# Optimization experiments

Hardware: AMD Instinct MI355X
Metric: run time of the kernel (lower is better)

## Reference

```python
import jax, jax.numpy as jnp
import numpy as np

C = 512
H = 8
D = C // H
GROUPS = 32
EPS = 1e-5

def setup_inputs() -> dict:
    key = jax.random.key(0)
    ks = jax.random.split(key, 7)
    B, L = 4, 2048
    x = jax.random.normal(ks[0], (B, C, L), dtype=jnp.float32)
    gamma = jnp.ones((C,), dtype=jnp.float32)
    beta = jnp.zeros((C,), dtype=jnp.float32)
    w_qkv = jax.random.normal(ks[1], (3 * C, C), dtype=jnp.float32) * (1.0 / np.sqrt(C))
    b_qkv = jax.random.normal(ks[2], (3 * C,), dtype=jnp.float32) * 0.01
    w_proj = jax.random.normal(ks[3], (C, C), dtype=jnp.float32) * (1.0 / np.sqrt(C))
    b_proj = jax.random.normal(ks[4], (C,), dtype=jnp.float32) * 0.01
    return {"x": x, "gamma": gamma, "beta": beta, "w_qkv": w_qkv,
            "b_qkv": b_qkv, "w_proj": w_proj, "b_proj": b_proj}

def _group_norm(x, gamma, beta):
    B, Cc, L = x.shape
    xg = x.reshape(B, GROUPS, Cc // GROUPS, L)
    mean = jnp.mean(xg, axis=(2, 3), keepdims=True)
    var = jnp.var(xg, axis=(2, 3), keepdims=True)
    xn = ((xg - mean) * jax.lax.rsqrt(var + EPS)).reshape(B, Cc, L)
    return xn * gamma[None, :, None] + beta[None, :, None]

def reference(x, gamma, beta, w_qkv, b_qkv, w_proj, b_proj):
    B, Cc, L = x.shape
    h = _group_norm(x, gamma, beta)
    # 1x1 conv == channel matmul: (3C,C) x (B,C,L) -> (B,3C,L)
    qkv = jnp.einsum('oc,bcl->bol', w_qkv, h) + b_qkv[None, :, None]
    q, k, v = jnp.split(qkv, 3, axis=1)
    # (B,C,L) -> (B,H,L,D)
    def to_heads(t):
        return t.reshape(B, H, D, L).transpose(0, 1, 3, 2)
    q, k, v = to_heads(q), to_heads(k), to_heads(v)
    scale = 1.0 / np.sqrt(D).astype(np.float32)
    attn = jnp.einsum('bhqd,bhkd->bhqk', q, k) * scale  # [B,H,L,L]
    attn = jax.nn.softmax(attn, axis=-1)
    out = jnp.einsum('bhqk,bhkd->bhqd', attn, v)  # [B,H,L,D]
    out = out.transpose(0, 1, 3, 2).reshape(B, Cc, L)
    proj = jnp.einsum('oc,bcl->bol', w_proj, out) + b_proj[None, :, None]
    return x + proj
```

## Files before the change

kernel.cpp:

```cpp
#include <hip/hip_runtime.h>
#include <stdint.h>

#define C_DIM 512
#define H_HEADS 8
#define D_HEAD 64
#define B_BATCH 4
#define L_SEQ 2048
#define GROUPS 32
#define EPS_GN 1e-5f

typedef unsigned short u16;
typedef __attribute__((ext_vector_type(8))) __bf16 bf16x8;
typedef __attribute__((ext_vector_type(4))) float f32x4;
typedef __attribute__((ext_vector_type(16))) float f32x16;

__device__ __forceinline__ u16 f2bf(float f) {
  unsigned u = __builtin_bit_cast(unsigned, f);
  unsigned r = u + 0x7FFFu + ((u >> 16) & 1u);
  return (u16)(r >> 16);
}

__device__ __forceinline__ unsigned cvtpk_bf16(float lo, float hi) {
  unsigned r;
  asm("v_cvt_pk_bf16_f32 %0, %1, %2" : "=v"(r) : "v"(lo), "v"(hi));
  return r;
}

__device__ __forceinline__ void pl32swap(unsigned& a, unsigned& b) {
  asm("v_permlane32_swap_b32 %0, %1" : "+v"(a), "+v"(b));
}

__device__ __forceinline__ bf16x8 mk8(unsigned a, unsigned b, unsigned c, unsigned d) {
  union { uint4 u; bf16x8 v; } z;
  z.u.x = a; z.u.y = b; z.u.z = c; z.u.w = d;
  return z.v;
}

__device__ __forceinline__ void gl16(const void* g, void* l) {
  __builtin_amdgcn_global_load_lds((const __attribute__((address_space(1))) void*)g,
                                   (__attribute__((address_space(3))) void*)l, 16, 0, 0);
}

__global__ __launch_bounds__(256) void cvt_weights(const float* __restrict__ wq,
                                                   const float* __restrict__ wp,
                                                   u16* __restrict__ wq_bf,
                                                   u16* __restrict__ wp_bf) {
  int i = blockIdx.x * 256 + threadIdx.x;
  const int nq = 3 * C_DIM * C_DIM;
  int idx = i * 4;
  const float* src;
  u16* dst;
  if (idx < nq) { src = wq + idx; dst = wq_bf + idx; }
  else          { src = wp + (idx - nq); dst = wp_bf + (idx - nq); }
  float4 v = *(const float4*)src;
  uint2 pk;
  pk.x = (unsigned)f2bf(v.x) | ((unsigned)f2bf(v.y) << 16);
  pk.y = (unsigned)f2bf(v.z) | ((unsigned)f2bf(v.w) << 16);
  *(uint2*)dst = pk;
}

__global__ __launch_bounds__(256) void groupnorm_kernel(const float* __restrict__ x,
                                                        const float* __restrict__ gamma,
                                                        const float* __restrict__ beta,
                                                        u16* __restrict__ h_t) {
  int bg = blockIdx.x;
  int b = bg >> 5, g = bg & 31;
  const float* base = x + ((size_t)(b * C_DIM + g * 16)) * L_SEQ;
  int t = threadIdx.x;
  int w = t >> 6;
  float s = 0.f, sq = 0.f;
  for (int i = 0; i < 32; ++i) {
    float4 v = ((const float4*)base)[t + i * 256];
    s += v.x + v.y + v.z + v.w;
    sq += v.x * v.x + v.y * v.y + v.z * v.z + v.w * v.w;
  }
  for (int off = 32; off; off >>= 1) { s += __shfl_down(s, off); sq += __shfl_down(sq, off); }
  __shared__ float red[8];
  if ((t & 63) == 0) { red[w * 2] = s; red[w * 2 + 1] = sq; }
  __syncthreads();
  float ts = red[0] + red[2] + red[4] + red[6];
  float tq = red[1] + red[3] + red[5] + red[7];
  float mean = ts * (1.f / 32768.f);
  float var = tq * (1.f / 32768.f) - mean * mean;
  float rstd = rsqrtf(var + EPS_GN);
  float ga[16], be[16];
#pragma unroll
  for (int c = 0; c < 16; ++c) {
    float gm = gamma[g * 16 + c];
    ga[c] = gm * rstd;
    be[c] = beta[g * 16 + c] - mean * gm * rstd;
  }
  __shared__ float tile[16][260];
  for (int lc = 0; lc < 8; ++lc) {
    __syncthreads();
#pragma unroll
    for (int it = 0; it < 4; ++it) {
      int r = it * 4 + w;
      int c4 = (t & 63) * 4;
      *(float4*)&tile[r][c4] = *(const float4*)(base + (size_t)r * L_SEQ + lc * 256 + c4);
    }
    __syncthreads();
    int l = lc * 256 + t;
    unsigned wds[8];
#pragma unroll
    for (int c = 0; c < 8; ++c) {
      float a0 = tile[2 * c][t] * ga[2 * c] + be[2 * c];
      float a1 = tile[2 * c + 1][t] * ga[2 * c + 1] + be[2 * c + 1];
      wds[c] = (unsigned)f2bf(a0) | ((unsigned)f2bf(a1) << 16);
    }
    u16* dst = h_t + ((size_t)(b * L_SEQ + l)) * C_DIM + g * 16;
    uint4 p0; p0.x = wds[0]; p0.y = wds[1]; p0.z = wds[2]; p0.w = wds[3];
    uint4 p1; p1.x = wds[4]; p1.y = wds[5]; p1.z = wds[6]; p1.w = wds[7];
    *(uint4*)dst = p0;
    *(uint4*)(dst + 8) = p1;
  }
}

template <int MODE>
__global__ __launch_bounds__(256) void gemm_kernel(const u16* __restrict__ A_bf,
                                                   const u16* __restrict__ B_t,
                                                   const float* __restrict__ bias,
                                                   const float* __restrict__ xres,
                                                   u16* __restrict__ q_t,
                                                   u16* __restrict__ kf_g,
                                                   u16* __restrict__ vf_g,
                                                   float* __restrict__ out_f) {
  constexpr int K = 512;
  __shared__ u16 A_lds[128][32];
  __shared__ u16 B_lds[128][32];
  int t = threadIdx.x;
  int w = t >> 6, lane = t & 63;
  int q4 = lane >> 4, c15 = lane & 15;
  int wm = w >> 1, wn = w & 1;
  int o0 = blockIdx.y * 128;
  int l0 = blockIdx.x * 128;
  int b = blockIdx.z;
  const u16* Bb = B_t + (size_t)b * L_SEQ * K;
  f32x4 acc[4][4] = {};

  int sr = lane >> 2, sc = lane & 3;
  int r0 = w * 32 + sr;
  int r1 = r0 + 16;
  int lc0 = (sc - (r0 >> 1)) & 3;
  int lc1 = (sc - (r1 >> 1)) & 3;
  const u16* Ag0 = A_bf + (size_t)(o0 + r0) * K + lc0 * 8;
  const u16* Ag1 = A_bf + (size_t)(o0 + r1) * K + lc1 * 8;
  const u16* Bg0 = Bb + (size_t)(l0 + r0) * K + lc0 * 8;
  const u16* Bg1 = Bb + (size_t)(l0 + r1) * K + lc1 * 8;
  u16* Al0 = &A_lds[w * 32][0];
  u16* Al1 = &A_lds[w * 32 + 16][0];
  u16* Bl0 = &B_lds[w * 32][0];
  u16* Bl1 = &B_lds[w * 32 + 16][0];

  for (int kt = 0; kt < K / 32; ++kt) {
    gl16(Ag0, Al0); gl16(Ag1, Al1);
    gl16(Bg0, Bl0); gl16(Bg1, Bl1);
    Ag0 += 32; Ag1 += 32; Bg0 += 32; Bg1 += 32;
    __syncthreads();
    bf16x8 af[4], bfr[4];
#pragma unroll
    for (int mi = 0; mi < 4; ++mi) {
      int ar = wm * 64 + mi * 16 + c15;
      af[mi] = *(const bf16x8*)&A_lds[ar][((q4 + (ar >> 1)) & 3) * 8];
    }
#pragma unroll
    for (int ni = 0; ni < 4; ++ni) {
      int br = wn * 64 + ni * 16 + c15;
      bfr[ni] = *(const bf16x8*)&B_lds[br][((q4 + (br >> 1)) & 3) * 8];
    }
#pragma unroll
    for (int mi = 0; mi < 4; ++mi)
#pragma unroll
      for (int ni = 0; ni < 4; ++ni)
        acc[mi][ni] = __builtin_amdgcn_mfma_f32_16x16x32_bf16(af[mi], bfr[ni], acc[mi][ni], 0, 0, 0);
    __syncthreads();
  }

  if (MODE == 0) {
    const float QS = 0.18033688f;
    int sel = o0 >> 9;
    int ob = o0 - sel * 512 + wm * 64;
#pragma unroll
    for (int mi = 0; mi < 4; ++mi) {
      int orow = ob + mi * 16 + q4 * 4;
      float4 bi = *(const float4*)&bias[o0 + wm * 64 + mi * 16 + q4 * 4];
#pragma unroll
      for (int ni = 0; ni < 4; ++ni) {
        int l = l0 + wn * 64 + ni * 16 + c15;
        float v0 = acc[mi][ni][0] + bi.x;
        float v1 = acc[mi][ni][1] + bi.y;
        float v2 = acc[mi][ni][2] + bi.z;
        float v3 = acc[mi][ni][3] + bi.w;
        if (sel == 0) {
          v0 *= QS; v1 *= QS; v2 *= QS; v3 *= QS;
          uint2 pk;
          pk.x = (unsigned)f2bf(v0) | ((unsigned)f2bf(v1) << 16);
          pk.y = (unsigned)f2bf(v2) | ((unsigned)f2bf(v3) << 16);
          *(uint2*)(q_t + ((size_t)(b * L_SEQ + l)) * C_DIM + orow) = pk;
        } else if (sel == 1) {
          int hh = orow >> 6, d = orow & 63;
          size_t base = ((size_t)(b * 8 + hh)) * 131072 +
                        (size_t)(((l >> 5) * 4 + (d >> 4))) * 512 +
                        (size_t)((l & 31) + ((d >> 3) & 1) * 32) * 8 + (d & 7);
          uint2 pk;
          pk.x = (unsigned)f2bf(v0) | ((unsigned)f2bf(v1) << 16);
          pk.y = (unsigned)f2bf(v2) | ((unsigned)f2bf(v3) << 16);
          *(uint2*)(kf_g + base) = pk;
        } else {
          int hh = orow >> 6, d = orow & 63;
          size_t base0 = ((size_t)(b * 8 + hh)) * 131072 +
                         (size_t)(l >> 4) * 1024 +
                         (size_t)((l >> 3) & 1) * 256 + (l & 7);
          vf_g[base0 + (size_t)((d + 0) >> 5) * 512 + ((d + 0) & 31) * 8] = f2bf(v0);
          vf_g[base0 + (size_t)((d + 1) >> 5) * 512 + ((d + 1) & 31) * 8] = f2bf(v1);
          vf_g[base0 + (size_t)((d + 2) >> 5) * 512 + ((d + 2) & 31) * 8] = f2bf(v2);
          vf_g[base0 + (size_t)((d + 3) >> 5) * 512 + ((d + 3) & 31) * 8] = f2bf(v3);
        }
      }
    }
  } else {
#pragma unroll
    for (int mi = 0; mi < 4; ++mi) {
      int orow = o0 + wm * 64 + mi * 16 + q4 * 4;
      float4 bi = *(const float4*)&bias[orow];
#pragma unroll
      for (int ni = 0; ni < 4; ++ni) {
        int l = l0 + wn * 64 + ni * 16 + c15;
        size_t base2 = ((size_t)(b * C_DIM + orow)) * L_SEQ + l;
        out_f[base2] = acc[mi][ni][0] + bi.x + xres[base2];
        out_f[base2 + L_SEQ] = acc[mi][ni][1] + bi.y + xres[base2 + L_SEQ];
        out_f[base2 + 2 * L_SEQ] = acc[mi][ni][2] + bi.z + xres[base2 + 2 * L_SEQ];
        out_f[base2 + 3 * L_SEQ] = acc[mi][ni][3] + bi.w + xres[base2 + 3 * L_SEQ];
      }
    }
  }
}

#define ABODY(KL, KN, VC, SC, SN, T)                                           \
  {                                                                            \
    int tl = (T) + 2; tl = tl > TMAX ? TMAX : tl;                              \
    const u16* kp = kfb + tl * 2048;                                           \
    const u16* vp = vfb + tl * 2048;                                           \
    KL[0] = *(const bf16x8*)(kp);                                              \
    KL[1] = *(const bf16x8*)(kp + 512);                                        \
    KL[2] = *(const bf16x8*)(kp + 1024);                                       \
    KL[3] = *(const bf16x8*)(kp + 1536);                                       \
    _Pragma("unroll") for (int r = 0; r < 16; ++r) SN[r] = 0.f;                \
    _Pragma("unroll") for (int kk = 0; kk < 4; ++kk)                           \
        SN = __builtin_amdgcn_mfma_f32_32x32x16_bf16(KN[kk], qf[kk], SN, 0, 0, 0); \
    float mx = fmaxf(fmaxf(SC[0], SC[1]), SC[2]);                              \
    float m1 = fmaxf(fmaxf(SC[3], SC[4]), SC[5]);                              \
    float m2 = fmaxf(fmaxf(SC[6], SC[7]), SC[8]);                              \
    float m3 = fmaxf(fmaxf(SC[9], SC[10]), SC[11]);                            \
    float m4 = fmaxf(fmaxf(SC[12], SC[13]), SC[14]);                           \
    mx = fmaxf(fmaxf(mx, SC[15]), fmaxf(m1, m2));                              \
    mx = fmaxf(mx, fmaxf(m3, m4));                                             \
    mx = fmaxf(mx, __shfl_xor(mx, 32));                                        \
    float mnew = fmaxf(m_r, mx);                                               \
    float al = __builtin_amdgcn_exp2f(m_r - mnew);                             \
    m_r = mnew;                                                                \
    l_r *= al;                                                                 \
    _Pragma("unroll") for (int r = 0; r < 16; ++r) { o0[r] *= al; o1[r] *= al; } \
    _Pragma("unroll") for (int r = 0; r < 16; ++r)                             \
        SC[r] = __builtin_amdgcn_exp2f(SC[r] - m_r);                           \
    float s0 = (SC[0] + SC[1]) + (SC[2] + SC[3]);                              \
    float s1 = (SC[4] + SC[5]) + (SC[6] + SC[7]);                              \
    float s2 = (SC[8] + SC[9]) + (SC[10] + SC[11]);                            \
    float s3 = (SC[12] + SC[13]) + (SC[14] + SC[15]);                          \
    float sum = (s0 + s1) + (s2 + s3);                                         \
    sum += __shfl_xor(sum, 32);                                                \
    l_r += sum;                                                                \
    unsigned pk[8];                                                            \
    _Pragma("unroll") for (int i = 0; i < 8; ++i)                              \
        pk[i] = cvtpk_bf16(SC[2 * i], SC[2 * i + 1]);                          \
    pl32swap(pk[0], pk[2]); pl32swap(pk[1], pk[3]);                            \
    pl32swap(pk[4], pk[6]); pl32swap(pk[5], pk[7]);                            \
    bf16x8 pf0 = mk8(pk[0], pk[1], pk[2], pk[3]);                              \
    bf16x8 pf1 = mk8(pk[4], pk[5], pk[6], pk[7]);                              \
    o0 = __builtin_amdgcn_mfma_f32_32x32x16_bf16(VC[0], pf0, o0, 0, 0, 0);     \
    o1 = __builtin_amdgcn_mfma_f32_32x32x16_bf16(VC[1], pf0, o1, 0, 0, 0);     \
    o0 = __builtin_amdgcn_mfma_f32_32x32x16_bf16(VC[2], pf1, o0, 0, 0, 0);     \
    o1 = __builtin_amdgcn_mfma_f32_32x32x16_bf16(VC[3], pf1, o1, 0, 0, 0);     \
    VC[0] = *(const bf16x8*)(vp);                                              \
    VC[1] = *(const bf16x8*)(vp + 512);                                        \
    VC[2] = *(const bf16x8*)(vp + 1024);                                       \
    VC[3] = *(const bf16x8*)(vp + 1536);                                       \
  }

#define AEPI(VC, SC)                                                           \
  {                                                                            \
    float mx = fmaxf(fmaxf(SC[0], SC[1]), SC[2]);                              \
    float m1 = fmaxf(fmaxf(SC[3], SC[4]), SC[5]);                              \
    float m2 = fmaxf(fmaxf(SC[6], SC[7]), SC[8]);                              \
    float m3 = fmaxf(fmaxf(SC[9], SC[10]), SC[11]);                            \
    float m4 = fmaxf(fmaxf(SC[12], SC[13]), SC[14]);                           \
    mx = fmaxf(fmaxf(mx, SC[15]), fmaxf(m1, m2));                              \
    mx = fmaxf(mx, fmaxf(m3, m4));                                             \
    mx = fmaxf(mx, __shfl_xor(mx, 32));                                        \
    float mnew = fmaxf(m_r, mx);                                               \
    float al = __builtin_amdgcn_exp2f(m_r - mnew);                             \
    m_r = mnew;                                                                \
    l_r *= al;                                                                 \
    _Pragma("unroll") for (int r = 0; r < 16; ++r) { o0[r] *= al; o1[r] *= al; } \
    _Pragma("unroll") for (int r = 0; r < 16; ++r)                             \
        SC[r] = __builtin_amdgcn_exp2f(SC[r] - m_r);                           \
    float s0 = (SC[0] + SC[1]) + (SC[2] + SC[3]);                              \
    float s1 = (SC[4] + SC[5]) + (SC[6] + SC[7]);                              \
    float s2 = (SC[8] + SC[9]) + (SC[10] + SC[11]);                            \
    float s3 = (SC[12] + SC[13]) + (SC[14] + SC[15]);                          \
    float sum = (s0 + s1) + (s2 + s3);                                         \
    sum += __shfl_xor(sum, 32);                                                \
    l_r += sum;                                                                \
    unsigned pk[8];                                                            \
    _Pragma("unroll") for (int i = 0; i < 8; ++i)                              \
        pk[i] = cvtpk_bf16(SC[2 * i], SC[2 * i + 1]);                          \
    pl32swap(pk[0], pk[2]); pl32swap(pk[1], pk[3]);                            \
    pl32swap(pk[4], pk[6]); pl32swap(pk[5], pk[7]);                            \
    bf16x8 pf0 = mk8(pk[0], pk[1], pk[2], pk[3]);                              \
    bf16x8 pf1 = mk8(pk[4], pk[5], pk[6], pk[7]);                              \
    o0 = __builtin_amdgcn_mfma_f32_32x32x16_bf16(VC[0], pf0, o0, 0, 0, 0);     \
    o1 = __builtin_amdgcn_mfma_f32_32x32x16_bf16(VC[1], pf0, o1, 0, 0, 0);     \
    o0 = __builtin_amdgcn_mfma_f32_32x32x16_bf16(VC[2], pf1, o0, 0, 0, 0);     \
    o1 = __builtin_amdgcn_mfma_f32_32x32x16_bf16(VC[3], pf1, o1, 0, 0, 0);     \
  }

__global__ __launch_bounds__(256, 3) void attn_kernel(const u16* __restrict__ q_t,
                                                      const u16* __restrict__ kf_g,
                                                      const u16* __restrict__ vf_g,
                                                      u16* __restrict__ ao_t) {
  __shared__ float oL[4][64][32];
  __shared__ float mL[4][32];
  __shared__ float lL[4][32];

  int g = blockIdx.x;
  int wk = (g & 7) * 256 + (g >> 3);
  int qg = wk & 63, bh = wk >> 6;
  int b = bh >> 3, h = bh & 7;
  int t = threadIdx.x;
  int wv = t >> 6, lane = t & 63;
  int q = lane & 31, hi = lane >> 5;
  int q0 = qg * 32;
  const int TMAX = 15;

  const u16* qp = q_t + ((size_t)(b * L_SEQ + q0 + q)) * C_DIM + h * 64 + hi * 8;
  bf16x8 qf[4];
#pragma unroll
  for (int kk = 0; kk < 4; ++kk) qf[kk] = *(const bf16x8*)(qp + kk * 16);

  const u16* kfb = kf_g + (size_t)bh * 131072 + (size_t)wv * 32768 + lane * 8;
  const u16* vfb = vf_g + (size_t)bh * 131072 + (size_t)wv * 32768 + lane * 8;

  f32x16 o0, o1;
#pragma unroll
  for (int r = 0; r < 16; ++r) { o0[r] = 0.f; o1[r] = 0.f; }
  float m_r = -1e30f, l_r = 0.f;

  bf16x8 kA[4], kB[4], vA[4], vB[4];
#pragma unroll
  for (int i = 0; i < 4; ++i) {
    kB[i] = *(const bf16x8*)(kfb + i * 512);
    kA[i] = *(const bf16x8*)(kfb + 2048 + i * 512);
    vA[i] = *(const bf16x8*)(vfb + i * 512);
    vB[i] = *(const bf16x8*)(vfb + 2048 + i * 512);
  }
  f32x16 sA, sB;
#pragma unroll
  for (int r = 0; r < 16; ++r) sA[r] = 0.f;
#pragma unroll
  for (int kk = 0; kk < 4; ++kk)
    sA = __builtin_amdgcn_mfma_f32_32x32x16_bf16(kB[kk], qf[kk], sA, 0, 0, 0);

  for (int it = 0; it < 7; ++it) {
    ABODY(kB, kA, vA, sA, sB, 2 * it);
    ABODY(kA, kB, vB, sB, sA, 2 * it + 1);
  }
  ABODY(kB, kA, vA, sA, sB, 14);
  AEPI(vB, sB);

  if (hi == 0) mL[wv][q] = m_r;
  __syncthreads();
  float ms = fmaxf(fmaxf(mL[0][q], mL[1][q]), fmaxf(mL[2][q], mL[3][q]));
  float scl = __builtin_amdgcn_exp2f(m_r - ms);
  if (hi == 0) lL[wv][q] = l_r * scl;
#pragma unroll
  for (int r = 0; r < 16; ++r) {
    int d = (r & 3) + 8 * (r >> 2) + 4 * hi;
    oL[wv][d][q] = o0[r] * scl;
    oL[wv][d + 32][q] = o1[r] * scl;
  }
  __syncthreads();

  int tq = t & 31;
  int dbase = (t >> 5) * 8;
  float lsum = (lL[0][tq] + lL[1][tq]) + (lL[2][tq] + lL[3][tq]);
  float inv = 1.f / lsum;
  float v[8];
#pragma unroll
  for (int i = 0; i < 8; ++i) {
    int d = dbase + i;
    v[i] = ((oL[0][d][tq] + oL[1][d][tq]) + (oL[2][d][tq] + oL[3][d][tq])) * inv;
  }
  uint4 ov;
  ov.x = cvtpk_bf16(v[0], v[1]);
  ov.y = cvtpk_bf16(v[2], v[3]);
  ov.z = cvtpk_bf16(v[4], v[5]);
  ov.w = cvtpk_bf16(v[6], v[7]);
  *(uint4*)(ao_t + ((size_t)(b * L_SEQ + q0 + tq)) * C_DIM + h * 64 + dbase) = ov;
}

extern "C" void kernel_launch(void* const* d_in, const int* in_sizes, int n_in,
                              void* d_out, int out_size, void* d_ws, size_t ws_size,
                              hipStream_t stream) {
  const float* x = (const float*)d_in[0];
  const float* gamma = (const float*)d_in[1];
  const float* beta = (const float*)d_in[2];
  const float* w_qkv = (const float*)d_in[3];
  const float* b_qkv = (const float*)d_in[4];
  const float* w_proj = (const float*)d_in[5];
  const float* b_proj = (const float*)d_in[6];
  float* out = (float*)d_out;

  u16* wq_bf = (u16*)d_ws;
  u16* wp_bf = wq_bf + 786432;
  u16* h_t = wp_bf + 262144;
  u16* q_t = h_t + 4194304;
  u16* kf_g = q_t + 4194304;
  u16* vf_g = kf_g + 4194304;
  u16* ao_t = vf_g + 4194304;

  cvt_weights<<<dim3(1024), dim3(256), 0, stream>>>(w_qkv, w_proj, wq_bf, wp_bf);
  groupnorm_kernel<<<dim3(128), dim3(256), 0, stream>>>(x, gamma, beta, h_t);
  gemm_kernel<0><<<dim3(16, 12, 4), dim3(256), 0, stream>>>(wq_bf, h_t, b_qkv, nullptr, q_t, kf_g, vf_g, nullptr);
  attn_kernel<<<dim3(2048), dim3(256), 0, stream>>>(q_t, kf_g, vf_g, ao_t);
  gemm_kernel<1><<<dim3(16, 4, 4), dim3(256), 0, stream>>>(wp_bf, ao_t, b_proj, x, nullptr, nullptr, nullptr, out);
}
```

Measured before the change: 116.8 us.

## Double-buffer GEMM LDS tiles and simplify attention loop with lazy rescaling

The GEMM kernel now double-buffers its A/B LDS tiles, prefetching the next K-slice while computing the current one, so one barrier per iteration replaces two. The attention kernel drops its hand-pipelined K/V register double-buffering in favour of a simple per-tile loop. That loop rescales the running max and output only when some lane's new max exceeds the old by more than 8 (log2 units), and launch bounds are raised to 4 blocks per CU for higher occupancy. The lazy rescale skips many exp and multiply ops, but the fp32 accumulators can grow by up to 2^8 before rescaling, and losing the software prefetch may expose global-load latency in attention.

Measured after the change: 118.2 us. No clear change (+1.2%).

```diff
diff --git a/kernel.cpp b/kernel.cpp
--- a/kernel.cpp
+++ b/kernel.cpp
@@ -126,8 +126,8 @@
                                                    u16* __restrict__ vf_g,
                                                    float* __restrict__ out_f) {
   constexpr int K = 512;
-  __shared__ u16 A_lds[128][32];
-  __shared__ u16 B_lds[128][32];
+  __shared__ u16 A_lds[2][128][32];
+  __shared__ u16 B_lds[2][128][32];
   int t = threadIdx.x;
   int w = t >> 6, lane = t & 63;
   int q4 = lane >> 4, c15 = lane & 15;
@@ -147,33 +147,42 @@
   const u16* Ag1 = A_bf + (size_t)(o0 + r1) * K + lc1 * 8;
   const u16* Bg0 = Bb + (size_t)(l0 + r0) * K + lc0 * 8;
   const u16* Bg1 = Bb + (size_t)(l0 + r1) * K + lc1 * 8;
-  u16* Al0 = &A_lds[w * 32][0];
-  u16* Al1 = &A_lds[w * 32 + 16][0];
-  u16* Bl0 = &B_lds[w * 32][0];
-  u16* Bl1 = &B_lds[w * 32 + 16][0];
+
+  gl16(Ag0, &A_lds[0][w * 32][0]);
+  gl16(Ag1, &A_lds[0][w * 32 + 16][0]);
+  gl16(Bg0, &B_lds[0][w * 32][0]);
+  gl16(Bg1, &B_lds[0][w * 32 + 16][0]);
+  Ag0 += 32; Ag1 += 32; Bg0 += 32; Bg1 += 32;
+  asm volatile("s_waitcnt vmcnt(0)" ::: "memory");
+  __builtin_amdgcn_s_barrier();
 
   for (int kt = 0; kt < K / 32; ++kt) {
-    gl16(Ag0, Al0); gl16(Ag1, Al1);
-    gl16(Bg0, Bl0); gl16(Bg1, Bl1);
-    Ag0 += 32; Ag1 += 32; Bg0 += 32; Bg1 += 32;
-    __syncthreads();
+    int cur = kt & 1, nxt = cur ^ 1;
+    if (kt < K / 32 - 1) {
+      gl16(Ag0, &A_lds[nxt][w * 32][0]);
+      gl16(Ag1, &A_lds[nxt][w * 32 + 16][0]);
+      gl16(Bg0, &B_lds[nxt][w * 32][0]);
+      gl16(Bg1, &B_lds[nxt][w * 32 + 16][0]);
+      Ag0 += 32; Ag1 += 32; Bg0 += 32; Bg1 += 32;
+    }
     bf16x8 af[4], bfr[4];
 #pragma unroll
     for (int mi = 0; mi < 4; ++mi) {
       int ar = wm * 64 + mi * 16 + c15;
-      af[mi] = *(const bf16x8*)&A_lds[ar][((q4 + (ar >> 1)) & 3) * 8];
+      af[mi] = *(const bf16x8*)&A_lds[cur][ar][((q4 + (ar >> 1)) & 3) * 8];
     }
 #pragma unroll
     for (int ni = 0; ni < 4; ++ni) {
       int br = wn * 64 + ni * 16 + c15;
-      bfr[ni] = *(const bf16x8*)&B_lds[br][((q4 + (br >> 1)) & 3) * 8];
+      bfr[ni] = *(const bf16x8*)&B_lds[cur][br][((q4 + (br >> 1)) & 3) * 8];
     }
 #pragma unroll
     for (int mi = 0; mi < 4; ++mi)
 #pragma unroll
       for (int ni = 0; ni < 4; ++ni)
         acc[mi][ni] = __builtin_amdgcn_mfma_f32_16x16x32_bf16(af[mi], bfr[ni], acc[mi][ni], 0, 0, 0);
-    __syncthreads();
+    asm volatile("s_waitcnt vmcnt(0)" ::: "memory");
+    __builtin_amdgcn_s_barrier();
   }
 
   if (MODE == 0) {
@@ -236,95 +245,7 @@
   }
 }
 
-#define ABODY(KL, KN, VC, SC, SN, T)                                           \
-  {                                                                            \
-    int tl = (T) + 2; tl = tl > TMAX ? TMAX : tl;                              \
-    const u16* kp = kfb + tl * 2048;                                           \
-    const u16* vp = vfb + tl * 2048;                                           \
-    KL[0] = *(const bf16x8*)(kp);                                              \
-    KL[1] = *(const bf16x8*)(kp + 512);                                        \
-    KL[2] = *(const bf16x8*)(kp + 1024);                                       \
-    KL[3] = *(const bf16x8*)(kp + 1536);                                       \
-    _Pragma("unroll") for (int r = 0; r < 16; ++r) SN[r] = 0.f;                \
-    _Pragma("unroll") for (int kk = 0; kk < 4; ++kk)                           \
-        SN = __builtin_amdgcn_mfma_f32_32x32x16_bf16(KN[kk], qf[kk], SN, 0, 0, 0); \
-    float mx = fmaxf(fmaxf(SC[0], SC[1]), SC[2]);                              \
-    float m1 = fmaxf(fmaxf(SC[3], SC[4]), SC[5]);                              \
-    float m2 = fmaxf(fmaxf(SC[6], SC[7]), SC[8]);                              \
-    float m3 = fmaxf(fmaxf(SC[9], SC[10]), SC[11]);                            \
-    float m4 = fmaxf(fmaxf(SC[12], SC[13]), SC[14]);                           \
-    mx = fmaxf(fmaxf(mx, SC[15]), fmaxf(m1, m2));                              \
-    mx = fmaxf(mx, fmaxf(m3, m4));                                             \
-    mx = fmaxf(mx, __shfl_xor(mx, 32));                                        \
-    float mnew = fmaxf(m_r, mx);                                               \
-    float al = __builtin_amdgcn_exp2f(m_r - mnew);                             \
-    m_r = mnew;                                                                \
-    l_r *= al;                                                                 \
-    _Pragma("unroll") for (int r = 0; r < 16; ++r) { o0[r] *= al; o1[r] *= al; } \
-    _Pragma("unroll") for (int r = 0; r < 16; ++r)                             \
-        SC[r] = __builtin_amdgcn_exp2f(SC[r] - m_r);                           \
-    float s0 = (SC[0] + SC[1]) + (SC[2] + SC[3]);                              \
-    float s1 = (SC[4] + SC[5]) + (SC[6] + SC[7]);                              \
-    float s2 = (SC[8] + SC[9]) + (SC[10] + SC[11]);                            \
-    float s3 = (SC[12] + SC[13]) + (SC[14] + SC[15]);                          \
-    float sum = (s0 + s1) + (s2 + s3);                                         \
-    sum += __shfl_xor(sum, 32);                                                \
-    l_r += sum;                                                                \
-    unsigned pk[8];                                                            \
-    _Pragma("unroll") for (int i = 0; i < 8; ++i)                              \
-        pk[i] = cvtpk_bf16(SC[2 * i], SC[2 * i + 1]);                          \
-    pl32swap(pk[0], pk[2]); pl32swap(pk[1], pk[3]);                            \
-    pl32swap(pk[4], pk[6]); pl32swap(pk[5], pk[7]);                            \
-    bf16x8 pf0 = mk8(pk[0], pk[1], pk[2], pk[3]);                              \
-    bf16x8 pf1 = mk8(pk[4], pk[5], pk[6], pk[7]);                              \
-    o0 = __builtin_amdgcn_mfma_f32_32x32x16_bf16(VC[0], pf0, o0, 0, 0, 0);     \
-    o1 = __builtin_amdgcn_mfma_f32_32x32x16_bf16(VC[1], pf0, o1, 0, 0, 0);     \
-    o0 = __builtin_amdgcn_mfma_f32_32x32x16_bf16(VC[2], pf1, o0, 0, 0, 0);     \
-    o1 = __builtin_amdgcn_mfma_f32_32x32x16_bf16(VC[3], pf1, o1, 0, 0, 0);     \
-    VC[0] = *(const bf16x8*)(vp);                                              \
-    VC[1] = *(const bf16x8*)(vp + 512);                                        \
-    VC[2] = *(const bf16x8*)(vp + 1024);                                       \
-    VC[3] = *(const bf16x8*)(vp + 1536);                                       \
-  }
-
-#define AEPI(VC, SC)                                                           \
-  {                                                                            \
-    float mx = fmaxf(fmaxf(SC[0], SC[1]), SC[2]);                              \
-    float m1 = fmaxf(fmaxf(SC[3], SC[4]), SC[5]);                              \
-    float m2 = fmaxf(fmaxf(SC[6], SC[7]), SC[8]);                              \
-    float m3 = fmaxf(fmaxf(SC[9], SC[10]), SC[11]);                            \
-    float m4 = fmaxf(fmaxf(SC[12], SC[13]), SC[14]);                           \
-    mx = fmaxf(fmaxf(mx, SC[15]), fmaxf(m1, m2));                              \
-    mx = fmaxf(mx, fmaxf(m3, m4));                                             \
-    mx = fmaxf(mx, __shfl_xor(mx, 32));                                        \
-    float mnew = fmaxf(m_r, mx);                                               \
-    float al = __builtin_amdgcn_exp2f(m_r - mnew);                             \
-    m_r = mnew;                                                                \
-    l_r *= al;                                                                 \
-    _Pragma("unroll") for (int r = 0; r < 16; ++r) { o0[r] *= al; o1[r] *= al; } \
-    _Pragma("unroll") for (int r = 0; r < 16; ++r)                             \
-        SC[r] = __builtin_amdgcn_exp2f(SC[r] - m_r);                           \
-    float s0 = (SC[0] + SC[1]) + (SC[2] + SC[3]);                              \
-    float s1 = (SC[4] + SC[5]) + (SC[6] + SC[7]);                              \
-    float s2 = (SC[8] + SC[9]) + (SC[10] + SC[11]);                            \
-    float s3 = (SC[12] + SC[13]) + (SC[14] + SC[15]);                          \
-    float sum = (s0 + s1) + (s2 + s3);                                         \
-    sum += __shfl_xor(sum, 32);                                                \
-    l_r += sum;                                                                \
-    unsigned pk[8];                                                            \
-    _Pragma("unroll") for (int i = 0; i < 8; ++i)                              \
-        pk[i] = cvtpk_bf16(SC[2 * i], SC[2 * i + 1]);                          \
-    pl32swap(pk[0], pk[2]); pl32swap(pk[1], pk[3]);                            \
-    pl32swap(pk[4], pk[6]); pl32swap(pk[5], pk[7]);                            \
-    bf16x8 pf0 = mk8(pk[0], pk[1], pk[2], pk[3]);                              \
-    bf16x8 pf1 = mk8(pk[4], pk[5], pk[6], pk[7]);                              \
-    o0 = __builtin_amdgcn_mfma_f32_32x32x16_bf16(VC[0], pf0, o0, 0, 0, 0);     \
-    o1 = __builtin_amdgcn_mfma_f32_32x32x16_bf16(VC[1], pf0, o1, 0, 0, 0);     \
-    o0 = __builtin_amdgcn_mfma_f32_32x32x16_bf16(VC[2], pf1, o0, 0, 0, 0);     \
-    o1 = __builtin_amdgcn_mfma_f32_32x32x16_bf16(VC[3], pf1, o1, 0, 0, 0);     \
-  }
-
-__global__ __launch_bounds__(256, 3) void attn_kernel(const u16* __restrict__ q_t,
+__global__ __launch_bounds__(256, 4) void attn_kernel(const u16* __restrict__ q_t,
                                                       const u16* __restrict__ kf_g,
                                                       const u16* __restrict__ vf_g,
                                                       u16* __restrict__ ao_t) {
@@ -340,7 +261,6 @@
   int wv = t >> 6, lane = t & 63;
   int q = lane & 31, hi = lane >> 5;
   int q0 = qg * 32;
-  const int TMAX = 15;
 
   const u16* qp = q_t + ((size_t)(b * L_SEQ + q0 + q)) * C_DIM + h * 64 + hi * 8;
   bf16x8 qf[4];
@@ -355,27 +275,64 @@
   for (int r = 0; r < 16; ++r) { o0[r] = 0.f; o1[r] = 0.f; }
   float m_r = -1e30f, l_r = 0.f;
 
-  bf16x8 kA[4], kB[4], vA[4], vB[4];
-#pragma unroll
-  for (int i = 0; i < 4; ++i) {
-    kB[i] = *(const bf16x8*)(kfb + i * 512);
-    kA[i] = *(const bf16x8*)(kfb + 2048 + i * 512);
-    vA[i] = *(const bf16x8*)(vfb + i * 512);
-    vB[i] = *(const bf16x8*)(vfb + 2048 + i * 512);
-  }
-  f32x16 sA, sB;
-#pragma unroll
-  for (int r = 0; r < 16; ++r) sA[r] = 0.f;
-#pragma unroll
-  for (int kk = 0; kk < 4; ++kk)
-    sA = __builtin_amdgcn_mfma_f32_32x32x16_bf16(kB[kk], qf[kk], sA, 0, 0, 0);
-
-  for (int it = 0; it < 7; ++it) {
-    ABODY(kB, kA, vA, sA, sB, 2 * it);
-    ABODY(kA, kB, vB, sB, sA, 2 * it + 1);
-  }
-  ABODY(kB, kA, vA, sA, sB, 14);
-  AEPI(vB, sB);
+  for (int tile = 0; tile < 16; ++tile) {
+    const u16* kp = kfb + tile * 2048;
+    const u16* vp = vfb + tile * 2048;
+    bf16x8 k0 = *(const bf16x8*)(kp);
+    bf16x8 k1 = *(const bf16x8*)(kp + 512);
+    bf16x8 k2 = *(const bf16x8*)(kp + 1024);
+    bf16x8 k3 = *(const bf16x8*)(kp + 1536);
+    f32x16 s;
+#pragma unroll
+    for (int r = 0; r < 16; ++r) s[r] = 0.f;
+    s = __builtin_amdgcn_mfma_f32_32x32x16_bf16(k0, qf[0], s, 0, 0, 0);
+    s = __builtin_amdgcn_mfma_f32_32x32x16_bf16(k1, qf[1], s, 0, 0, 0);
+    s = __builtin_amdgcn_mfma_f32_32x32x16_bf16(k2, qf[2], s, 0, 0, 0);
+    s = __builtin_amdgcn_mfma_f32_32x32x16_bf16(k3, qf[3], s, 0, 0, 0);
+    bf16x8 v0 = *(const bf16x8*)(vp);
+    bf16x8 v1 = *(const bf16x8*)(vp + 512);
+    bf16x8 v2 = *(const bf16x8*)(vp + 1024);
+    bf16x8 v3 = *(const bf16x8*)(vp + 1536);
+
+    float mx = fmaxf(fmaxf(s[0], s[1]), s[2]);
+    float m1_ = fmaxf(fmaxf(s[3], s[4]), s[5]);
+    float m2_ = fmaxf(fmaxf(s[6], s[7]), s[8]);
+    float m3_ = fmaxf(fmaxf(s[9], s[10]), s[11]);
+    float m4_ = fmaxf(fmaxf(s[12], s[13]), s[14]);
+    mx = fmaxf(fmaxf(mx, s[15]), fmaxf(m1_, m2_));
+    mx = fmaxf(mx, fmaxf(m3_, m4_));
+    mx = fmaxf(mx, __shfl_xor(mx, 32));
+    if (__any(mx > m_r + 8.f)) {
+      float mnew = fmaxf(m_r, mx);
+      float al = __builtin_amdgcn_exp2f(m_r - mnew);
+      l_r *= al;
+#pragma unroll
+      for (int r = 0; r < 16; ++r) { o0[r] *= al; o1[r] *= al; }
+      m_r = mnew;
+    }
+#pragma unroll
+    for (int r = 0; r < 16; ++r) s[r] = __builtin_amdgcn_exp2f(s[r] - m_r);
+    float s0_ = (s[0] + s[1]) + (s[2] + s[3]);
+    float s1_ = (s[4] + s[5]) + (s[6] + s[7]);
+    float s2_ = (s[8] + s[9]) + (s[10] + s[11]);
+    float s3_ = (s[12] + s[13]) + (s[14] + s[15]);
+    float sum = (s0_ + s1_) + (s2_ + s3_);
+    sum += __shfl_xor(sum, 32);
+    l_r += sum;
+
+    unsigned pk[8];
+#pragma unroll
+    for (int i = 0; i < 8; ++i) pk[i] = cvtpk_bf16(s[2 * i], s[2 * i + 1]);
+    pl32swap(pk[0], pk[2]); pl32swap(pk[1], pk[3]);
+    pl32swap(pk[4], pk[6]); pl32swap(pk[5], pk[7]);
+    bf16x8 pf0 = mk8(pk[0], pk[1], pk[2], pk[3]);
+    bf16x8 pf1 = mk8(pk[4], pk[5], pk[6], pk[7]);
+
+    o0 = __builtin_amdgcn_mfma_f32_32x32x16_bf16(v0, pf0, o0, 0, 0, 0);
+    o1 = __builtin_amdgcn_mfma_f32_32x32x16_bf16(v1, pf0, o1, 0, 0, 0);
+    o0 = __builtin_amdgcn_mfma_f32_32x32x16_bf16(v2, pf1, o0, 0, 0, 0);
+    o1 = __builtin_amdgcn_mfma_f32_32x32x16_bf16(v3, pf1, o1, 0, 0, 0);
+  }
 
   if (hi == 0) mL[wv][q] = m_r;
   __syncthreads();
```
